# Performance work log

Hardware: AMD Instinct MI355X
Metric: run time of the kernel (lower is better)

Reference implementation:

```python
import jax, jax.numpy as jnp
import numpy as np

N = 50000
F_IN = 128
E = 800000
C = 32      # hidden_channels
H1 = 8      # heads_1
H2 = 1      # heads_2
NEG_SLOPE = 0.2


def setup_inputs() -> dict:
    key = jax.random.key(0)
    ks = jax.random.split(key, 16)
    s = 0.1
    x = jax.random.normal(ks[0], (N, F_IN), dtype=jnp.float32)
    edge_index = jax.random.randint(ks[1], (2, E), 0, N, dtype=jnp.int32)
    # layer 1: in=F_IN, out=C, heads=H1, concat=True
    Wl1 = jax.random.normal(ks[2], (H1 * C, F_IN), dtype=jnp.float32) * s
    bl1 = jnp.zeros((H1 * C,), dtype=jnp.float32)
    Wr1 = jax.random.normal(ks[3], (H1 * C, F_IN), dtype=jnp.float32) * s
    br1 = jnp.zeros((H1 * C,), dtype=jnp.float32)
    att1 = jax.random.normal(ks[4], (H1, C), dtype=jnp.float32) * s
    bias1 = jnp.zeros((H1 * C,), dtype=jnp.float32)
    # layer 2: in=H1*C, out=C, heads=H2, concat=False (mean)
    Wl2 = jax.random.normal(ks[5], (H2 * C, H1 * C), dtype=jnp.float32) * s
    bl2 = jnp.zeros((H2 * C,), dtype=jnp.float32)
    Wr2 = jax.random.normal(ks[6], (H2 * C, H1 * C), dtype=jnp.float32) * s
    br2 = jnp.zeros((H2 * C,), dtype=jnp.float32)
    att2 = jax.random.normal(ks[7], (H2, C), dtype=jnp.float32) * s
    bias2 = jnp.zeros((C,), dtype=jnp.float32)
    return {"x": x, "edge_index": edge_index,
            "Wl1": Wl1, "bl1": bl1, "Wr1": Wr1, "br1": br1, "att1": att1, "bias1": bias1,
            "Wl2": Wl2, "bl2": bl2, "Wr2": Wr2, "br2": br2, "att2": att2, "bias2": bias2}


def _gatv2_layer(x, src, dst, Wl, bl, Wr, br, att, bias, heads, out_c, concat):
    n = x.shape[0]
    xl = (x @ Wl.T + bl).reshape(n, heads, out_c)  # source transform
    xr = (x @ Wr.T + br).reshape(n, heads, out_c)  # target transform
    z = jax.nn.leaky_relu(xl[src] + xr[dst], NEG_SLOPE)          # [E, H, C]
    logit = jnp.einsum('ehc,hc->eh', z, att)                     # [E, H]
    # segment softmax over incoming edges of each target node
    m = jax.ops.segment_max(logit, dst, num_segments=n)          # [N, H]
    ex = jnp.exp(logit - m[dst])
    denom = jax.ops.segment_sum(ex, dst, num_segments=n)
    alpha = ex / jnp.maximum(denom[dst], 1e-16)                  # [E, H]
    out = jax.ops.segment_sum(alpha[..., None] * xl[src], dst, num_segments=n)  # [N, H, C]
    out = out.reshape(n, heads * out_c) if concat else out.mean(axis=1)
    return out + bias


def reference(x, edge_index, Wl1, bl1, Wr1, br1, att1, bias1,
              Wl2, bl2, Wr2, br2, att2, bias2):
    n = x.shape[0]
    # PyG GATv2Conv default: add self loops
    loops = jnp.arange(n, dtype=edge_index.dtype)
    src = jnp.concatenate([edge_index[0], loops])
    dst = jnp.concatenate([edge_index[1], loops])
    h = _gatv2_layer(x, src, dst, Wl1, bl1, Wr1, br1, att1, bias1, H1, C, True)
    h = jax.nn.gelu(h, approximate=False)
    out = _gatv2_layer(h, src, dst, Wl2, bl2, Wr2, br2, att2, bias2, H2, C, False)
    return out
```

## Files before the change

### kernel.cpp

```cpp
#include <hip/hip_runtime.h>
#include <hip/hip_bf16.h>


typedef unsigned short u16;
typedef short bf16x8 __attribute__((ext_vector_type(8)));
typedef float f32x4 __attribute__((ext_vector_type(4)));
typedef float f32x2 __attribute__((ext_vector_type(2)));

#define F_IN   128
#define CH     32
#define H1     8
#define JT1    512
#define JH1    256
#define JT2    64
#define JH2    32

#define OFF_Y1     0UL
#define OFF_H      52000000UL
#define OFF_Y2     78000000UL
#define OFF_COL    85000000UL
#define OFF_DEG    89000000UL
#define OFF_ROW    89400000UL
#define OFF_CUR    89800000UL
#define OFF_WC     90200000UL
#define OFF_FLAG   90600000UL
#define OFF_BSUM   90700000UL
#define WS_NEED    91000000UL

#define W_WL1   0
#define W_BL1   32768
#define W_WR1   33024
#define W_BR1   65792
#define W_ATT1  66048
#define W_BIAS1 66304
#define W_WL2   66560
#define W_BL2   74752
#define W_WR2   74784
#define W_BR2   82976
#define W_ATT2  83008
#define W_BIAS2 83040
#define W_TOTAL 83072

__device__ inline float b2f(u16 u) { return __uint_as_float(((unsigned)u) << 16); }
__device__ inline u16 f2b(float f) {
    unsigned u = __float_as_uint(f);
    unsigned r = (u + 0x7fffu + ((u >> 16) & 1u)) >> 16;
    return (u16)r;
}
__device__ inline unsigned cvtpk(float lo, float hi) {
    unsigned r;
    asm("v_cvt_pk_bf16_f32 %0, %1, %2" : "=v"(r) : "v"(lo), "v"(hi));
    return r;
}
__device__ inline f32x2 pk_add(f32x2 a, f32x2 b) {
    f32x2 d;
    asm("v_pk_add_f32 %0, %1, %2" : "=v"(d) : "v"(a), "v"(b));
    return d;
}
__device__ inline f32x2 pk_fma(f32x2 a, f32x2 b, f32x2 c) {
    f32x2 d;
    asm("v_pk_fma_f32 %0, %1, %2, %3" : "=v"(d) : "v"(a), "v"(b), "v"(c));
    return d;
}
__device__ inline f32x2 unpk(unsigned u) {
    f32x2 d;
    d.x = __uint_as_float(u << 16);
    d.y = __uint_as_float(u & 0xffff0000u);
    return d;
}
__device__ inline f32x2 pabs(f32x2 z) {
    f32x2 d;
    d.x = __uint_as_float(__float_as_uint(z.x) & 0x7fffffffu);
    d.y = __uint_as_float(__float_as_uint(z.y) & 0x7fffffffu);
    return d;
}

struct WcArgs { const void* src[12]; int cum[13]; };

__global__ __launch_bounds__(256) void prep(
    WcArgs a, const u16* __restrict__ xprobe, u16* __restrict__ dst, int total,
    int* __restrict__ flagOut, int NBW,
    const int* __restrict__ ei, int* __restrict__ deg, int E_, int NP) {
    const int t = threadIdx.x;
    if ((int)blockIdx.x >= NBW) {
        int e = ((int)blockIdx.x - NBW) * 256 + t;
        if (e >= E_ + NP) return;
        int dstn = (e < E_) ? ei[E_ + e] : e - E_;
        atomicAdd(deg + dstn, 1);
        return;
    }
    __shared__ int cnt[256];
    __shared__ int sflag;
    int c = 0;
    for (int i = t; i < 512; i += 256) {
        u16 u = xprobe[i];
        int e = (u >> 7) & 0xff;
        c += (u == 0 || (e >= 100 && e <= 141)) ? 1 : 0;
    }
    cnt[t] = c; __syncthreads();
    for (int off = 128; off; off >>= 1) {
        if (t < off) cnt[t] += cnt[t + off];
        __syncthreads();
    }
    if (t == 0) {
        sflag = (cnt[0] >= 440) ? 1 : 0;
        if (blockIdx.x == 0) *flagOut = sflag;
    }
    __syncthreads();
    const int fl = sflag;
    int i = blockIdx.x * 256 + t;
    if (i >= total) return;
    int s = 0;
    while (i >= a.cum[s + 1]) s++;
    int rel = i - a.cum[s];
    if (fl) dst[i] = ((const u16*)a.src[s])[rel];
    else    dst[i] = f2b(((const float*)a.src[s])[rel]);
}

__global__ __launch_bounds__(256) void scan_part(const int* __restrict__ deg,
                                                 int* __restrict__ bsum, int NN) {
    __shared__ int red[256];
    int b = blockIdx.x, t = threadIdx.x;
    int base = b * 1024 + t * 4;
    int s = 0;
#pragma unroll
    for (int j = 0; j < 4; j++) { int i = base + j; if (i < NN) s += deg[i]; }
    red[t] = s; __syncthreads();
    for (int off = 128; off; off >>= 1) {
        if (t < off) red[t] += red[t + off];
        __syncthreads();
    }
    if (t == 0) bsum[b] = red[0];
}

__global__ __launch_bounds__(256) void scan_final(
    const int* __restrict__ deg, const int* __restrict__ bsum,
    int* __restrict__ rowptr, int* __restrict__ cur, int NN, int NB) {
    __shared__ int sb[256];
    __shared__ int ps[256];
    int b = blockIdx.x, t = threadIdx.x;
    int bv = (t < NB) ? bsum[t] : 0;
    sb[t] = bv; __syncthreads();
    for (int off = 1; off < 256; off <<= 1) {
        int x = (t >= off) ? sb[t - off] : 0;
        __syncthreads();
        sb[t] += x;
        __syncthreads();
    }
    if (b == 0 && t == 0) rowptr[NN] = sb[NB - 1];
    int boff = (b == 0) ? 0 : sb[b - 1];

    int base = b * 1024 + t * 4;
    int v[4]; int s = 0;
#pragma unroll
    for (int j = 0; j < 4; j++) { int i = base + j; v[j] = (i < NN) ? deg[i] : 0; s += v[j]; }
    ps[t] = s; __syncthreads();
    for (int off = 1; off < 256; off <<= 1) {
        int x = (t >= off) ? ps[t - off] : 0;
        __syncthreads();
        ps[t] += x;
        __syncthreads();
    }
    int run = boff + (t ? ps[t - 1] : 0);
#pragma unroll
    for (int j = 0; j < 4; j++) {
        int i = base + j;
        if (i < NN) { rowptr[i] = run; cur[i] = run; run += v[j]; }
    }
}

__global__ void scatter_edges(const int* __restrict__ ei, int* __restrict__ cur,
                              int* __restrict__ col, int E_, int NP) {
    int e = blockIdx.x * 256 + threadIdx.x;
    if (e >= E_ + NP) return;
    int src, dst;
    if (e < E_) { src = ei[e]; dst = ei[E_ + e]; }
    else        { src = dst = e - E_; }
    int pos = atomicAdd(cur + dst, 1);
    col[pos] = src;
}

template <int K, bool DYN>
__global__ __launch_bounds__(256) void gemm_mfma(
    const void* __restrict__ X, const u16* __restrict__ Wl, const u16* __restrict__ Wr,
    const u16* __restrict__ bl, const u16* __restrict__ br,
    u16* __restrict__ Y, int M, int JH, const int* __restrict__ flagp) {
    __shared__ float cs[4][32][68];
    const int t = threadIdx.x, w = t >> 6, l = t & 63;
    const int bm0 = blockIdx.x * 128, bn0 = blockIdx.y * 64;
    const int JT = 2 * JH;
    const int lr = l & 15, lk = (l >> 4) * 8;
    const int fl = DYN ? *flagp : 1;

    int rowm[2];
#pragma unroll
    for (int mt = 0; mt < 2; mt++) {
        int row = bm0 + w * 32 + mt * 16 + lr;
        if (row >= M) row = M - 1;
        rowm[mt] = row;
    }

    constexpr int KK = K / 32;
    bf16x8 afr[2][KK];
    if (fl) {
        const u16* xb = (const u16*)X;
#pragma unroll
        for (int mt = 0; mt < 2; mt++)
#pragma unroll
            for (int kk = 0; kk < KK; kk++)
                afr[mt][kk] = *(const bf16x8*)(xb + (size_t)rowm[mt] * K + lk + kk * 32);
    } else {
        const float* xf = (const float*)X;
#pragma unroll
        for (int mt = 0; mt < 2; mt++)
#pragma unroll
            for (int kk = 0; kk < KK; kk++) {
                const float* p = xf + (size_t)rowm[mt] * K + lk + kk * 32;
                float4 v0 = *(const float4*)p;
                float4 v1 = *(const float4*)(p + 4);
                uint4 o;
                o.x = cvtpk(v0.x, v0.y); o.y = cvtpk(v0.z, v0.w);
                o.z = cvtpk(v1.x, v1.y); o.w = cvtpk(v1.z, v1.w);
                afr[mt][kk] = *(bf16x8*)&o;
            }
    }

    const u16* bx[4];
    float bv[4];
#pragma unroll
    for (int nt = 0; nt < 4; nt++) {
        int j = bn0 + nt * 16 + lr;
        const u16* wp = (j < JH) ? (Wl + (size_t)j * K) : (Wr + (size_t)(j - JH) * K);
        bx[nt] = wp + lk;
        bv[nt] = b2f(j < JH ? bl[j] : br[j - JH]);
    }

    f32x4 acc[2][4];
#pragma unroll
    for (int mt = 0; mt < 2; mt++)
#pragma unroll
        for (int nt = 0; nt < 4; nt++) acc[mt][nt] = (f32x4){0.f, 0.f, 0.f, 0.f};

#pragma unroll
    for (int kk = 0; kk < KK; kk++) {
        bf16x8 b[4];
#pragma unroll
        for (int nt = 0; nt < 4; nt++) b[nt] = *(const bf16x8*)(bx[nt] + kk * 32);
#pragma unroll
        for (int mt = 0; mt < 2; mt++)
#pragma unroll
            for (int nt = 0; nt < 4; nt++)
                acc[mt][nt] = __builtin_amdgcn_mfma_f32_16x16x32_bf16(
                    afr[mt][kk], b[nt], acc[mt][nt], 0, 0, 0);
    }

#pragma unroll
    for (int mt = 0; mt < 2; mt++)
#pragma unroll
        for (int nt = 0; nt < 4; nt++)
#pragma unroll
            for (int r = 0; r < 4; r++)
                cs[w][mt * 16 + (l >> 4) * 4 + r][nt * 16 + lr] = acc[mt][nt][r] + bv[nt];

#pragma unroll
    for (int p = 0; p < 4; p++) {
        int rl = p * 8 + (l >> 3);
        int grow = bm0 + w * 32 + rl;
        if (grow < M) {
            const float* rp = &cs[w][rl][(l & 7) * 8];
            float4 v0 = *(const float4*)rp;
            float4 v1 = *(const float4*)(rp + 4);
            uint4 o;
            o.x = cvtpk(v0.x, v0.y); o.y = cvtpk(v0.z, v0.w);
            o.z = cvtpk(v1.x, v1.y); o.w = cvtpk(v1.z, v1.w);
            *(uint4*)(Y + (size_t)grow * JT + bn0 + (l & 7) * 8) = o;
        }
    }
}

__global__ __launch_bounds__(256, 4) void agg1(
    const u16* __restrict__ Y1, const int* __restrict__ rowptr,
    const int* __restrict__ col, const u16* __restrict__ att,
    const u16* __restrict__ bias, u16* __restrict__ hout, int NN) {
    const int wid = blockIdx.x * 4 + (threadIdx.x >> 6);
    if (wid >= NN) return;
    const int lane = threadIdx.x & 63, half = lane >> 5, hl = lane & 31;
    const int n = wid;

    f32x2 xr2[4], a06[4], a04[4];
    {
        uint4 rx = *(const uint4*)(Y1 + (size_t)n * JT1 + JH1 + hl * 8);
        uint4 ra = *(const uint4*)(att + hl * 8);
        unsigned ux[4] = {rx.x, rx.y, rx.z, rx.w};
        unsigned ua[4] = {ra.x, ra.y, ra.z, ra.w};
#pragma unroll
        for (int p = 0; p < 4; p++) {
            xr2[p] = unpk(ux[p]);
            f32x2 a = unpk(ua[p]);
            a06[p].x = 0.6f * a.x; a06[p].y = 0.6f * a.y;
            a04[p].x = 0.4f * a.x; a04[p].y = 0.4f * a.y;
        }
    }
    f32x2 acc2[4] = {{0.f,0.f},{0.f,0.f},{0.f,0.f},{0.f,0.f}};
    float dsum = 0.f;

    auto edge = [&](uint4 raw) {
        unsigned uw[4] = {raw.x, raw.y, raw.z, raw.w};
        f32x2 xl2[4];
        f32x2 p2 = {0.f, 0.f};
#pragma unroll
        for (int p = 0; p < 4; p++) {
            xl2[p] = unpk(uw[p]);
            f32x2 z = pk_add(xl2[p], xr2[p]);
            p2 = pk_fma(z, a06[p], p2);
            p2 = pk_fma(pabs(z), a04[p], p2);
        }
        float pl = p2.x + p2.y;
        pl += __shfl_xor(pl, 1); pl += __shfl_xor(pl, 2);
        float e = __expf(pl);
        dsum += e;
        f32x2 e2; e2.x = e; e2.y = e;
#pragma unroll
        for (int p = 0; p < 4; p++) acc2[p] = pk_fma(e2, xl2[p], acc2[p]);
    };

    const int beg = rowptr[n], end = rowptr[n + 1];
    int i = beg + half;
    for (; i + 14 < end; i += 16) {
        int s[8];
#pragma unroll
        for (int k = 0; k < 8; k++) s[k] = col[i + 2 * k];
        uint4 r[8];
#pragma unroll
        for (int k = 0; k < 8; k++) r[k] = *(const uint4*)(Y1 + (size_t)s[k] * JT1 + hl * 8);
#pragma unroll
        for (int k = 0; k < 8; k++) edge(r[k]);
    }
    for (; i + 6 < end; i += 8) {
        int s0 = col[i], s1 = col[i + 2], s2 = col[i + 4], s3 = col[i + 6];
        uint4 r0 = *(const uint4*)(Y1 + (size_t)s0 * JT1 + hl * 8);
        uint4 r1 = *(const uint4*)(Y1 + (size_t)s1 * JT1 + hl * 8);
        uint4 r2 = *(const uint4*)(Y1 + (size_t)s2 * JT1 + hl * 8);
        uint4 r3 = *(const uint4*)(Y1 + (size_t)s3 * JT1 + hl * 8);
        edge(r0); edge(r1); edge(r2); edge(r3);
    }
    for (; i < end; i += 2) {
        uint4 r0 = *(const uint4*)(Y1 + (size_t)col[i] * JT1 + hl * 8);
        edge(r0);
    }

    dsum += __shfl_xor(dsum, 32);
#pragma unroll
    for (int p = 0; p < 4; p++) {
        acc2[p].x += __shfl_xor(acc2[p].x, 32);
        acc2[p].y += __shfl_xor(acc2[p].y, 32);
    }

    if (half == 0) {
        float inv = 1.f / fmaxf(dsum, 1e-16f);
        u16 bu[8];
        *(uint4*)bu = *(const uint4*)(bias + hl * 8);
        float v[8];
#pragma unroll
        for (int p = 0; p < 4; p++) {
            float x0 = acc2[p].x * inv + b2f(bu[2 * p]);
            float x1 = acc2[p].y * inv + b2f(bu[2 * p + 1]);
            v[2 * p]     = 0.5f * x0 * (1.f + erff(x0 * 0.70710678118654752f));
            v[2 * p + 1] = 0.5f * x1 * (1.f + erff(x1 * 0.70710678118654752f));
        }
        uint4 o;
        o.x = cvtpk(v[0], v[1]); o.y = cvtpk(v[2], v[3]);
        o.z = cvtpk(v[4], v[5]); o.w = cvtpk(v[6], v[7]);
        *(uint4*)(hout + (size_t)n * JH1 + hl * 8) = o;
    }
}

__global__ __launch_bounds__(256) void agg2(
    const u16* __restrict__ Y2, const int* __restrict__ rowptr,
    const int* __restrict__ col, const u16* __restrict__ att,
    const u16* __restrict__ bias, void* __restrict__ dout, int NN,
    const int* __restrict__ flag) {
    const int wid = blockIdx.x * 4 + (threadIdx.x >> 6);
    if (wid >= NN) return;
    const int lane = threadIdx.x & 63, le = lane >> 4, cl = lane & 15;
    const int n = wid;

    f32x2 xr2 = unpk(*(const unsigned*)(Y2 + (size_t)n * JT2 + JH2 + cl * 2));
    f32x2 av  = unpk(*(const unsigned*)(att + cl * 2));
    f32x2 a06; a06.x = 0.6f * av.x; a06.y = 0.6f * av.y;
    f32x2 a04; a04.x = 0.4f * av.x; a04.y = 0.4f * av.y;
    f32x2 acc2 = {0.f, 0.f};
    float dsum = 0.f;

    auto edge = [&](unsigned raw, bool act) {
        f32x2 xl2 = unpk(raw);
        f32x2 z = pk_add(xl2, xr2);
        f32x2 p2 = pk_fma(z, a06, (f32x2){0.f, 0.f});
        p2 = pk_fma(pabs(z), a04, p2);
        float pl = p2.x + p2.y;
        pl += __shfl_xor(pl, 1); pl += __shfl_xor(pl, 2);
        pl += __shfl_xor(pl, 4); pl += __shfl_xor(pl, 8);
        float e = __expf(pl);
        if (!act) e = 0.f;
        dsum += e;
        f32x2 e2; e2.x = e; e2.y = e;
        acc2 = pk_fma(e2, xl2, acc2);
    };

    const int beg = rowptr[n], end = rowptr[n + 1];
    int i = beg;
    for (; i + 8 <= end; i += 8) {
        int sA = col[i + le];
        int sB = col[i + 4 + le];
        unsigned rA = *(const unsigned*)(Y2 + (size_t)sA * JT2 + cl * 2);
        unsigned rB = *(const unsigned*)(Y2 + (size_t)sB * JT2 + cl * 2);
        edge(rA, true);
        edge(rB, true);
    }
    for (; i < end; i += 4) {
        int idx = i + le;
        bool act = idx < end;
        int s0 = col[act ? idx : end - 1];
        unsigned r0 = *(const unsigned*)(Y2 + (size_t)s0 * JT2 + cl * 2);
        edge(r0, act);
    }

    dsum += __shfl_xor(dsum, 16); dsum += __shfl_xor(dsum, 32);
    acc2.x += __shfl_xor(acc2.x, 16); acc2.x += __shfl_xor(acc2.x, 32);
    acc2.y += __shfl_xor(acc2.y, 16); acc2.y += __shfl_xor(acc2.y, 32);

    if (le == 0) {
        float inv = 1.f / fmaxf(dsum, 1e-16f);
        f32x2 bv = unpk(*(const unsigned*)(bias + cl * 2));
        float v0 = acc2.x * inv + bv.x;
        float v1 = acc2.y * inv + bv.y;
        if (*flag) {
            *(unsigned*)((u16*)dout + n * JH2 + cl * 2) = cvtpk(v0, v1);
        } else {
            float2 o; o.x = v0; o.y = v1;
            *(float2*)((float*)dout + n * JH2 + cl * 2) = o;
        }
    }
}

extern "C" void kernel_launch(void* const* d_in, const int* in_sizes, int n_in,
                              void* d_out, int out_size, void* d_ws, size_t ws_size,
                              hipStream_t stream) {
    const int NN = in_sizes[0] / F_IN;
    const int EE = in_sizes[1] / 2;
    const int EP = EE + NN;
    if (ws_size < WS_NEED) return;

    char* w = (char*)d_ws;
    u16*   Y1   = (u16*)(w + OFF_Y1);
    u16*   hbuf = (u16*)(w + OFF_H);
    u16*   Y2   = (u16*)(w + OFF_Y2);
    int*   col  = (int*)(w + OFF_COL);
    int*   deg  = (int*)(w + OFF_DEG);
    int*   rowp = (int*)(w + OFF_ROW);
    int*   cur  = (int*)(w + OFF_CUR);
    u16*   Wc   = (u16*)(w + OFF_WC);
    int*   flag = (int*)(w + OFF_FLAG);
    int*   bsum = (int*)(w + OFF_BSUM);

    const int* ei = (const int*)d_in[1];

    hipMemsetAsync(deg, 0, (size_t)NN * 4, stream);
    {
        WcArgs a;
        int sizes[12] = {JH1 * F_IN, JH1, JH1 * F_IN, JH1, H1 * CH, JH1,
                         JH2 * JH1, JH2, JH2 * JH1, JH2, JH2, JH2};
        int c = 0;
        for (int s = 0; s < 12; s++) { a.src[s] = d_in[2 + s]; a.cum[s] = c; c += sizes[s]; }
        a.cum[12] = c;
        const int NBW = (W_TOTAL + 255) / 256;
        const int NBE = (EP + 255) / 256;
        prep<<<NBW + NBE, 256, 0, stream>>>(a, (const u16*)d_in[0], Wc, W_TOTAL,
                                            flag, NBW, ei, deg, EE, NN);
    }

    const int NB = (NN + 1023) / 1024;
    scan_part<<<NB, 256, 0, stream>>>(deg, bsum, NN);
    scan_final<<<NB, 256, 0, stream>>>(deg, bsum, rowp, cur, NN, NB);
    scatter_edges<<<(EP + 255) / 256, 256, 0, stream>>>(ei, cur, col, EE, NN);

    {
        dim3 grid((NN + 127) / 128, JT1 / 64);
        gemm_mfma<F_IN, true><<<grid, 256, 0, stream>>>(
            d_in[0], Wc + W_WL1, Wc + W_WR1, Wc + W_BL1, Wc + W_BR1, Y1, NN, JH1, flag);
    }
    agg1<<<(NN + 3) / 4, 256, 0, stream>>>(Y1, rowp, col, Wc + W_ATT1,
                                           Wc + W_BIAS1, hbuf, NN);

    {
        dim3 grid((NN + 127) / 128, JT2 / 64);
        gemm_mfma<JH1, false><<<grid, 256, 0, stream>>>(
            hbuf, Wc + W_WL2, Wc + W_WR2, Wc + W_BL2, Wc + W_BR2, Y2, NN, JH2, flag);
    }
    agg2<<<(NN + 3) / 4, 256, 0, stream>>>(Y2, rowp, col, Wc + W_ATT2,
                                           Wc + W_BIAS2, d_out, NN, flag);
}
```

Before: 278.6 us.

## Fuse edge scatter into layer-1 GEMM launch and loop column tiles per block

Edge scattering into CSR columns now runs inside the layer-1 GEMM launch, with extra blocks past the GEMM blocks doing the scatter, so one kernel launch is removed and the two independent jobs overlap. Each GEMM block now loops over all column groups and reuses its loaded A fragments, instead of using a 2D grid that reloads X per column tile. Layer-2 aggregation adds a 16-edge unrolled loop to keep more gathers in flight. The trade-off is fewer GEMM blocks, each doing more serial work, which lowers parallelism for layer 1.

```diff
diff --git a/kernel.cpp b/kernel.cpp
--- a/kernel.cpp
+++ b/kernel.cpp
@@ -169,25 +169,13 @@
     }
 }
 
-__global__ void scatter_edges(const int* __restrict__ ei, int* __restrict__ cur,
-                              int* __restrict__ col, int E_, int NP) {
-    int e = blockIdx.x * 256 + threadIdx.x;
-    if (e >= E_ + NP) return;
-    int src, dst;
-    if (e < E_) { src = ei[e]; dst = ei[E_ + e]; }
-    else        { src = dst = e - E_; }
-    int pos = atomicAdd(cur + dst, 1);
-    col[pos] = src;
-}
-
-template <int K, bool DYN>
-__global__ __launch_bounds__(256) void gemm_mfma(
+template <int K, int NG, bool DYN>
+__device__ __forceinline__ void gemm_body(
+    float (*cs)[32][68],
     const void* __restrict__ X, const u16* __restrict__ Wl, const u16* __restrict__ Wr,
     const u16* __restrict__ bl, const u16* __restrict__ br,
-    u16* __restrict__ Y, int M, int JH, const int* __restrict__ flagp) {
-    __shared__ float cs[4][32][68];
+    u16* __restrict__ Y, int M, int JH, const int* __restrict__ flagp, int bm0) {
     const int t = threadIdx.x, w = t >> 6, l = t & 63;
-    const int bm0 = blockIdx.x * 128, bn0 = blockIdx.y * 64;
     const int JT = 2 * JH;
     const int lr = l & 15, lk = (l >> 4) * 8;
     const int fl = DYN ? *flagp : 1;
@@ -225,57 +213,91 @@
             }
     }
 
-    const u16* bx[4];
-    float bv[4];
-#pragma unroll
-    for (int nt = 0; nt < 4; nt++) {
-        int j = bn0 + nt * 16 + lr;
-        const u16* wp = (j < JH) ? (Wl + (size_t)j * K) : (Wr + (size_t)(j - JH) * K);
-        bx[nt] = wp + lk;
-        bv[nt] = b2f(j < JH ? bl[j] : br[j - JH]);
-    }
-
-    f32x4 acc[2][4];
-#pragma unroll
-    for (int mt = 0; mt < 2; mt++)
-#pragma unroll
-        for (int nt = 0; nt < 4; nt++) acc[mt][nt] = (f32x4){0.f, 0.f, 0.f, 0.f};
-
-#pragma unroll
-    for (int kk = 0; kk < KK; kk++) {
-        bf16x8 b[4];
-#pragma unroll
-        for (int nt = 0; nt < 4; nt++) b[nt] = *(const bf16x8*)(bx[nt] + kk * 32);
+#pragma unroll 1
+    for (int g = 0; g < NG; g++) {
+        const int bn0 = g * 64;
+        const u16* bx[4];
+        float bv[4];
+#pragma unroll
+        for (int nt = 0; nt < 4; nt++) {
+            int j = bn0 + nt * 16 + lr;
+            const u16* wp = (j < JH) ? (Wl + (size_t)j * K) : (Wr + (size_t)(j - JH) * K);
+            bx[nt] = wp + lk;
+            bv[nt] = b2f(j < JH ? bl[j] : br[j - JH]);
+        }
+
+        f32x4 acc[2][4];
 #pragma unroll
         for (int mt = 0; mt < 2; mt++)
 #pragma unroll
+            for (int nt = 0; nt < 4; nt++) acc[mt][nt] = (f32x4){0.f, 0.f, 0.f, 0.f};
+
+#pragma unroll
+        for (int kk = 0; kk < KK; kk++) {
+            bf16x8 b[4];
+#pragma unroll
+            for (int nt = 0; nt < 4; nt++) b[nt] = *(const bf16x8*)(bx[nt] + kk * 32);
+#pragma unroll
+            for (int mt = 0; mt < 2; mt++)
+#pragma unroll
+                for (int nt = 0; nt < 4; nt++)
+                    acc[mt][nt] = __builtin_amdgcn_mfma_f32_16x16x32_bf16(
+                        afr[mt][kk], b[nt], acc[mt][nt], 0, 0, 0);
+        }
+
+#pragma unroll
+        for (int mt = 0; mt < 2; mt++)
+#pragma unroll
             for (int nt = 0; nt < 4; nt++)
-                acc[mt][nt] = __builtin_amdgcn_mfma_f32_16x16x32_bf16(
-                    afr[mt][kk], b[nt], acc[mt][nt], 0, 0, 0);
-    }
-
-#pragma unroll
-    for (int mt = 0; mt < 2; mt++)
-#pragma unroll
-        for (int nt = 0; nt < 4; nt++)
-#pragma unroll
-            for (int r = 0; r < 4; r++)
-                cs[w][mt * 16 + (l >> 4) * 4 + r][nt * 16 + lr] = acc[mt][nt][r] + bv[nt];
-
-#pragma unroll
-    for (int p = 0; p < 4; p++) {
-        int rl = p * 8 + (l >> 3);
-        int grow = bm0 + w * 32 + rl;
-        if (grow < M) {
-            const float* rp = &cs[w][rl][(l & 7) * 8];
-            float4 v0 = *(const float4*)rp;
-            float4 v1 = *(const float4*)(rp + 4);
-            uint4 o;
-            o.x = cvtpk(v0.x, v0.y); o.y = cvtpk(v0.z, v0.w);
-            o.z = cvtpk(v1.x, v1.y); o.w = cvtpk(v1.z, v1.w);
-            *(uint4*)(Y + (size_t)grow * JT + bn0 + (l & 7) * 8) = o;
-        }
-    }
+#pragma unroll
+                for (int r = 0; r < 4; r++)
+                    cs[w][mt * 16 + (l >> 4) * 4 + r][nt * 16 + lr] = acc[mt][nt][r] + bv[nt];
+
+#pragma unroll
+        for (int p = 0; p < 4; p++) {
+            int rl = p * 8 + (l >> 3);
+            int grow = bm0 + w * 32 + rl;
+            if (grow < M) {
+                const float* rp = &cs[w][rl][(l & 7) * 8];
+                float4 v0 = *(const float4*)rp;
+                float4 v1 = *(const float4*)(rp + 4);
+                uint4 o;
+                o.x = cvtpk(v0.x, v0.y); o.y = cvtpk(v0.z, v0.w);
+                o.z = cvtpk(v1.x, v1.y); o.w = cvtpk(v1.z, v1.w);
+                *(uint4*)(Y + (size_t)grow * JT + bn0 + (l & 7) * 8) = o;
+            }
+        }
+    }
+}
+
+__global__ __launch_bounds__(256) void gemm1_scatter(
+    const void* __restrict__ X, const u16* __restrict__ Wl, const u16* __restrict__ Wr,
+    const u16* __restrict__ bl, const u16* __restrict__ br,
+    u16* __restrict__ Y, int M, const int* __restrict__ flagp, int NBG,
+    const int* __restrict__ ei, int* __restrict__ cur, int* __restrict__ col,
+    int E_, int NP) {
+    __shared__ float cs[4][32][68];
+    if ((int)blockIdx.x < NBG) {
+        gemm_body<F_IN, JT1 / 64, true>(cs, X, Wl, Wr, bl, br, Y, M, JH1, flagp,
+                                        (int)blockIdx.x * 128);
+        return;
+    }
+    int e = ((int)blockIdx.x - NBG) * 256 + threadIdx.x;
+    if (e >= E_ + NP) return;
+    int src, dst;
+    if (e < E_) { src = ei[e]; dst = ei[E_ + e]; }
+    else        { src = dst = e - E_; }
+    int pos = atomicAdd(cur + dst, 1);
+    col[pos] = src;
+}
+
+__global__ __launch_bounds__(256) void gemm2_k(
+    const u16* __restrict__ X, const u16* __restrict__ Wl, const u16* __restrict__ Wr,
+    const u16* __restrict__ bl, const u16* __restrict__ br,
+    u16* __restrict__ Y, int M, const int* __restrict__ flagp) {
+    __shared__ float cs[4][32][68];
+    gemm_body<JH1, JT2 / 64, false>(cs, X, Wl, Wr, bl, br, Y, M, JH2, flagp,
+                                    (int)blockIdx.x * 128);
 }
 
 __global__ __launch_bounds__(256, 4) void agg1(
@@ -409,6 +431,15 @@
 
     const int beg = rowptr[n], end = rowptr[n + 1];
     int i = beg;
+    for (; i + 16 <= end; i += 16) {
+        int s0 = col[i + le], s1 = col[i + 4 + le];
+        int s2 = col[i + 8 + le], s3 = col[i + 12 + le];
+        unsigned r0 = *(const unsigned*)(Y2 + (size_t)s0 * JT2 + cl * 2);
+        unsigned r1 = *(const unsigned*)(Y2 + (size_t)s1 * JT2 + cl * 2);
+        unsigned r2 = *(const unsigned*)(Y2 + (size_t)s2 * JT2 + cl * 2);
+        unsigned r3 = *(const unsigned*)(Y2 + (size_t)s3 * JT2 + cl * 2);
+        edge(r0, true); edge(r1, true); edge(r2, true); edge(r3, true);
+    }
     for (; i + 8 <= end; i += 8) {
         int sA = col[i + le];
         int sB = col[i + 4 + le];
@@ -482,21 +513,19 @@
     const int NB = (NN + 1023) / 1024;
     scan_part<<<NB, 256, 0, stream>>>(deg, bsum, NN);
     scan_final<<<NB, 256, 0, stream>>>(deg, bsum, rowp, cur, NN, NB);
-    scatter_edges<<<(EP + 255) / 256, 256, 0, stream>>>(ei, cur, col, EE, NN);
 
     {
-        dim3 grid((NN + 127) / 128, JT1 / 64);
-        gemm_mfma<F_IN, true><<<grid, 256, 0, stream>>>(
-            d_in[0], Wc + W_WL1, Wc + W_WR1, Wc + W_BL1, Wc + W_BR1, Y1, NN, JH1, flag);
+        const int NBG = (NN + 127) / 128;
+        const int NBE = (EP + 255) / 256;
+        gemm1_scatter<<<NBG + NBE, 256, 0, stream>>>(
+            d_in[0], Wc + W_WL1, Wc + W_WR1, Wc + W_BL1, Wc + W_BR1,
+            Y1, NN, flag, NBG, ei, cur, col, EE, NN);
     }
     agg1<<<(NN + 3) / 4, 256, 0, stream>>>(Y1, rowp, col, Wc + W_ATT1,
                                            Wc + W_BIAS1, hbuf, NN);
 
-    {
-        dim3 grid((NN + 127) / 128, JT2 / 64);
-        gemm_mfma<JH1, false><<<grid, 256, 0, stream>>>(
-            hbuf, Wc + W_WL2, Wc + W_WR2, Wc + W_BL2, Wc + W_BR2, Y2, NN, JH2, flag);
-    }
+    gemm2_k<<<(NN + 127) / 128, 256, 0, stream>>>(
+        hbuf, Wc + W_WL2, Wc + W_WR2, Wc + W_BL2, Wc + W_BR2, Y2, NN, flag);
     agg2<<<(NN + 3) / 4, 256, 0, stream>>>(Y2, rowp, col, Wc + W_ATT2,
                                            Wc + W_BIAS2, d_out, NN, flag);
 }
```

New measurement: 250.6 us. -10.1%, faster.
